# Kernel optimization log

Measured on AMD Instinct MI355X. Metric: run time of the kernel, lower is better.

The kernel has to match this reference:

```python
import jax, jax.numpy as jnp
import numpy as np

DEPTH = 4  # truncation depth of the signature


def setup_inputs() -> dict:
    key = jax.random.key(0)
    # path: (batch, stream, channels)
    path = jax.random.normal(key, (128, 128, 12), dtype=jnp.float32)
    return {"path": path}


def _exp_terms(d, depth):
    """Tensor exponential of a single linear increment d: (B, C).

    Returns a tuple of flattened levels; level k has shape (B, C**k) and
    equals d^{\otimes k} / k!.
    """
    B = d.shape[0]
    terms = [d]
    for k in range(2, depth + 1):
        terms.append(jnp.einsum('bi,bj->bij', terms[-1], d).reshape(B, -1) / k)
    return tuple(terms)


def _signature(path, depth):
    """Truncated path signature (stream=False, basepoint=False).

    Combines per-increment tensor exponentials with Chen's identity:
    (A \otimes B)_m = A_m + B_m + sum_{i=1}^{m-1} A_i \otimes B_{m-i}.
    """
    B, L, C = path.shape
    dx = path[:, 1:] - path[:, :-1]  # (B, L-1, C) path increments
    init = _exp_terms(dx[:, 0], depth)

    def step(sig, d):
        e = _exp_terms(d, depth)
        new = []
        for m in range(1, depth + 1):  # signature level m, shape (B, C**m)
            t = sig[m - 1] + e[m - 1]
            for i in range(1, m):  # cross terms sig_i (x) e_{m-i}
                t = t + jnp.einsum('bi,bj->bij', sig[i - 1], e[m - i - 1]).reshape(B, -1)
            new.append(t)
        return tuple(new), None

    # scan over the remaining L-2 increments (time-major)
    sig, _ = jax.lax.scan(step, init, jnp.transpose(dx[:, 1:], (1, 0, 2)))
    # flatten levels in order 1..depth, matching signatory's layout
    return jnp.concatenate(sig, axis=-1)  # (B, C + C^2 + ... + C^depth)


def reference(path):
    return _signature(path, DEPTH)
```

## Files before the change

kernel.cpp:

```cpp
#include <hip/hip_runtime.h>


#define NC    12
#define NPTS  128
#define NSTEP 128
#define OUT_PER_B 22620
#define BT 448
#define PADQ 33

__global__ __launch_bounds__(BT)
void sig_kernel(const float* __restrict__ path, float* __restrict__ out) {
    const int bid = blockIdx.x;
    const int b  = bid >> 1;
    const int ih = bid & 1;
    const int t  = threadIdx.x;

    __shared__ __align__(16) float  P[NPTS * NC];
    __shared__ __align__(16) float  W[NSTEP * NC];
    __shared__ __align__(16) float4 DT4[NC * PADQ];

    const float* pb = path + (size_t)b * (NPTS * NC);
    if (t < 384) ((float4*)P)[t] = ((const float4*)pb)[t];
    __syncthreads();

    if (t < 384) {
        const int c  = t >> 5;
        const int sq = t & 31;
        float d[4];
        #pragma unroll
        for (int e = 0; e < 4; ++e) {
            const int s = 4 * sq + e;
            d[e] = (s < NPTS - 1) ? (P[(s + 1) * NC + c] - P[s * NC + c]) : 0.f;
            W[s * NC + c] = d[e];
        }
        DT4[c * PADQ + sq] = make_float4(d[0], d[1], d[2], d[3]);
    }
    __syncthreads();

    const int ta  = (t < 432) ? t : (t - 432);
    const int il  = ta / 72;
    const int rem = ta - il * 72;
    const int j   = rem / 6;
    const int kh  = rem - j * 6;
    const int i   = ih * 6 + il;
    const int k0  = kh * 2;

    float acc0[12], acc1[12];
    #pragma unroll
    for (int l = 0; l < 12; ++l) { acc0[l] = 0.f; acc1[l] = 0.f; }
    float s3a = 0.f, s3b = 0.f, s2 = 0.f, s1 = 0.f;

    const float4* wt   = (const float4*)W;
    const float4* dti  = &DT4[i * PADQ];
    const float4* dtj  = &DT4[j * PADQ];
    const float4* dtka = &DT4[k0 * PADQ];
    const float4* dtkb = &DT4[(k0 + 1) * PADQ];

    for (int sq = 0; sq < NSTEP / 4; ++sq) {
        float4 wq[12];
        #pragma unroll
        for (int q = 0; q < 12; ++q) wq[q] = wt[sq * 12 + q];

        float4 di4  = dti[sq];
        float4 dj4  = dtj[sq];
        float4 dka4 = dtka[sq];
        float4 dkb4 = dtkb[sq];

        #pragma unroll
        for (int u = 0; u < 4; ++u) {
            const float di  = (&di4.x)[u];
            const float dj  = (&dj4.x)[u];
            const float dka = (&dka4.x)[u];
            const float dkb = (&dkb4.x)[u];

            float A4  = (s1 + 0.25f * di) * (1.f / 3.f);
            float B4  = (s2 + dj * A4) * 0.5f;
            float C3a = s3a + dka * B4;
            float C3b = s3b + dkb * B4;

            #pragma unroll
            for (int l = 0; l < 12; ++l) {
                const float wl = (&wq[3 * u + (l >> 2)].x)[l & 3];
                acc0[l] += C3a * wl;
                acc1[l] += C3b * wl;
            }

            float A3 = (s1 + di * (1.f / 3.f)) * 0.5f;
            float C2 = s2 + dj * A3;
            s3a += dka * C2;
            s3b += dkb * C2;
            s2  += dj * (s1 + 0.5f * di);
            s1  += di;
        }
    }

    if (t < 432) {
        float* ob = out + (size_t)b * OUT_PER_B;
        if (j == 0 && kh == 0) ob[i] = s1;
        if (kh == 0) ob[12 + i * 12 + j] = s2;
        const int ijk = (i * 12 + j) * 12 + k0;
        ob[156 + ijk]     = s3a;
        ob[156 + ijk + 1] = s3b;
        float4* o4 = (float4*)(ob + 1884 + (size_t)ijk * 12);
        o4[0] = make_float4(acc0[0], acc0[1], acc0[2],  acc0[3]);
        o4[1] = make_float4(acc0[4], acc0[5], acc0[6],  acc0[7]);
        o4[2] = make_float4(acc0[8], acc0[9], acc0[10], acc0[11]);
        o4[3] = make_float4(acc1[0], acc1[1], acc1[2],  acc1[3]);
        o4[4] = make_float4(acc1[4], acc1[5], acc1[6],  acc1[7]);
        o4[5] = make_float4(acc1[8], acc1[9], acc1[10], acc1[11]);
    }
}

extern "C" void kernel_launch(void* const* d_in, const int* in_sizes, int n_in,
                              void* d_out, int out_size, void* d_ws, size_t ws_size,
                              hipStream_t stream) {
    const float* path = (const float*)d_in[0];
    float* out = (float*)d_out;
    const int nbatch = in_sizes[0] / (NPTS * NC);

    sig_kernel<<<nbatch * 2, BT, 0, stream>>>(path, out);
}
```

Measured before the change: 73.47 us.

## Widen per-thread k tile to four and double-buffer shared-memory loads

Each thread now handles four k indices instead of two, so the block shrinks from 448 to 256 threads and each W/increment load from shared memory feeds twice as many FMAs. The step loop is manually double-buffered, prefetching the next quad of increments into registers while the current one is computed. The cost is much higher register pressure (48 accumulators plus two 12-float4 buffers), which may lower occupancy or cause spills. The longer serial chain per thread also leaves fewer waves to hide latency.

```diff
diff --git a/kernel.cpp b/kernel.cpp
--- a/kernel.cpp
+++ b/kernel.cpp
@@ -3,9 +3,8 @@
 
 #define NC    12
 #define NPTS  128
-#define NSTEP 128
 #define OUT_PER_B 22620
-#define BT 448
+#define BT 256
 #define PADQ 33
 
 __global__ __launch_bounds__(BT)
@@ -16,98 +15,128 @@
     const int t  = threadIdx.x;
 
     __shared__ __align__(16) float  P[NPTS * NC];
-    __shared__ __align__(16) float  W[NSTEP * NC];
+    __shared__ __align__(16) float  W[NPTS * NC];
     __shared__ __align__(16) float4 DT4[NC * PADQ];
 
-    const float* pb = path + (size_t)b * (NPTS * NC);
-    if (t < 384) ((float4*)P)[t] = ((const float4*)pb)[t];
-    __syncthreads();
-
-    if (t < 384) {
-        const int c  = t >> 5;
-        const int sq = t & 31;
-        float d[4];
-        #pragma unroll
-        for (int e = 0; e < 4; ++e) {
-            const int s = 4 * sq + e;
-            d[e] = (s < NPTS - 1) ? (P[(s + 1) * NC + c] - P[s * NC + c]) : 0.f;
-            W[s * NC + c] = d[e];
-        }
-        DT4[c * PADQ + sq] = make_float4(d[0], d[1], d[2], d[3]);
+    {
+        const float4* pb4 = (const float4*)(path + (size_t)b * (NPTS * NC));
+        ((float4*)P)[t] = pb4[t];
+        if (t < 128) ((float4*)P)[t + 256] = pb4[t + 256];
     }
     __syncthreads();
 
-    const int ta  = (t < 432) ? t : (t - 432);
-    const int il  = ta / 72;
-    const int rem = ta - il * 72;
-    const int j   = rem / 6;
-    const int kh  = rem - j * 6;
+    #pragma unroll
+    for (int pass = 0; pass < 2; ++pass) {
+        const int idx = t + pass * 256;
+        if (idx < 384) {
+            const int c  = idx >> 5;
+            const int sq = idx & 31;
+            float d[4];
+            #pragma unroll
+            for (int e = 0; e < 4; ++e) {
+                const int s = 4 * sq + e;
+                d[e] = (s < NPTS - 1) ? (P[(s + 1) * NC + c] - P[s * NC + c]) : 0.f;
+                W[s * NC + c] = d[e];
+            }
+            DT4[c * PADQ + sq] = make_float4(d[0], d[1], d[2], d[3]);
+        }
+    }
+    __syncthreads();
+
+    const int ta  = (t < 216) ? t : (t - 216);
+    const int il  = ta / 36;
+    const int rem = ta - il * 36;
+    const int j   = rem / 3;
+    const int kq  = rem - j * 3;
     const int i   = ih * 6 + il;
-    const int k0  = kh * 2;
+    const int k0  = kq * 4;
 
-    float acc0[12], acc1[12];
+    float acc[4][12];
     #pragma unroll
-    for (int l = 0; l < 12; ++l) { acc0[l] = 0.f; acc1[l] = 0.f; }
-    float s3a = 0.f, s3b = 0.f, s2 = 0.f, s1 = 0.f;
+    for (int m = 0; m < 4; ++m)
+        #pragma unroll
+        for (int l = 0; l < 12; ++l) acc[m][l] = 0.f;
+    float s1 = 0.f, s2 = 0.f;
+    float s3[4] = {0.f, 0.f, 0.f, 0.f};
 
     const float4* wt   = (const float4*)W;
     const float4* dti  = &DT4[i * PADQ];
     const float4* dtj  = &DT4[j * PADQ];
-    const float4* dtka = &DT4[k0 * PADQ];
-    const float4* dtkb = &DT4[(k0 + 1) * PADQ];
+    const float4* dtk0 = &DT4[(k0 + 0) * PADQ];
+    const float4* dtk1 = &DT4[(k0 + 1) * PADQ];
+    const float4* dtk2 = &DT4[(k0 + 2) * PADQ];
+    const float4* dtk3 = &DT4[(k0 + 3) * PADQ];
 
-    for (int sq = 0; sq < NSTEP / 4; ++sq) {
-        float4 wq[12];
-        #pragma unroll
-        for (int q = 0; q < 12; ++q) wq[q] = wt[sq * 12 + q];
+    float4 wqA[12], wqB[12];
+    float4 trA[6],  trB[6];
 
-        float4 di4  = dti[sq];
-        float4 dj4  = dtj[sq];
-        float4 dka4 = dtka[sq];
-        float4 dkb4 = dtkb[sq];
+#define LOADBUF(WQ, TR, S) do {                                   \
+        _Pragma("unroll")                                         \
+        for (int q = 0; q < 12; ++q) WQ[q] = wt[(S) * 12 + q];    \
+        TR[0] = dti[S];  TR[1] = dtj[S];                          \
+        TR[2] = dtk0[S]; TR[3] = dtk1[S];                         \
+        TR[4] = dtk2[S]; TR[5] = dtk3[S];                         \
+    } while (0)
 
-        #pragma unroll
-        for (int u = 0; u < 4; ++u) {
-            const float di  = (&di4.x)[u];
-            const float dj  = (&dj4.x)[u];
-            const float dka = (&dka4.x)[u];
-            const float dkb = (&dkb4.x)[u];
+#define COMPUTE(WQ, TR) do {                                      \
+        _Pragma("unroll")                                         \
+        for (int u = 0; u < 4; ++u) {                             \
+            const float di  = (&TR[0].x)[u];                      \
+            const float dj  = (&TR[1].x)[u];                      \
+            const float dk0_ = (&TR[2].x)[u];                     \
+            const float dk1_ = (&TR[3].x)[u];                     \
+            const float dk2_ = (&TR[4].x)[u];                     \
+            const float dk3_ = (&TR[5].x)[u];                     \
+            float A4 = (s1 + 0.25f * di) * (1.f / 3.f);           \
+            float B4 = (s2 + dj * A4) * 0.5f;                     \
+            float C3_0 = s3[0] + dk0_ * B4;                       \
+            float C3_1 = s3[1] + dk1_ * B4;                       \
+            float C3_2 = s3[2] + dk2_ * B4;                       \
+            float C3_3 = s3[3] + dk3_ * B4;                       \
+            _Pragma("unroll")                                     \
+            for (int l = 0; l < 12; ++l) {                        \
+                const float wl = (&WQ[3 * u + (l >> 2)].x)[l & 3];\
+                acc[0][l] += C3_0 * wl;                           \
+                acc[1][l] += C3_1 * wl;                           \
+                acc[2][l] += C3_2 * wl;                           \
+                acc[3][l] += C3_3 * wl;                           \
+            }                                                     \
+            float A3 = (s1 + di * (1.f / 3.f)) * 0.5f;            \
+            float C2 = s2 + dj * A3;                              \
+            s3[0] += dk0_ * C2;                                   \
+            s3[1] += dk1_ * C2;                                   \
+            s3[2] += dk2_ * C2;                                   \
+            s3[3] += dk3_ * C2;                                   \
+            s2 += dj * (s1 + 0.5f * di);                          \
+            s1 += di;                                             \
+        }                                                         \
+    } while (0)
 
-            float A4  = (s1 + 0.25f * di) * (1.f / 3.f);
-            float B4  = (s2 + dj * A4) * 0.5f;
-            float C3a = s3a + dka * B4;
-            float C3b = s3b + dkb * B4;
-
-            #pragma unroll
-            for (int l = 0; l < 12; ++l) {
-                const float wl = (&wq[3 * u + (l >> 2)].x)[l & 3];
-                acc0[l] += C3a * wl;
-                acc1[l] += C3b * wl;
-            }
-
-            float A3 = (s1 + di * (1.f / 3.f)) * 0.5f;
-            float C2 = s2 + dj * A3;
-            s3a += dka * C2;
-            s3b += dkb * C2;
-            s2  += dj * (s1 + 0.5f * di);
-            s1  += di;
-        }
+    LOADBUF(wqA, trA, 0);
+    for (int sq = 0; sq < 32; sq += 2) {
+        LOADBUF(wqB, trB, sq + 1);
+        COMPUTE(wqA, trA);
+        if (sq + 2 < 32) LOADBUF(wqA, trA, sq + 2);
+        COMPUTE(wqB, trB);
     }
 
-    if (t < 432) {
+#undef LOADBUF
+#undef COMPUTE
+
+    if (t < 216) {
         float* ob = out + (size_t)b * OUT_PER_B;
-        if (j == 0 && kh == 0) ob[i] = s1;
-        if (kh == 0) ob[12 + i * 12 + j] = s2;
+        if (j == 0 && kq == 0) ob[i] = s1;
+        if (kq == 0) ob[12 + i * 12 + j] = s2;
         const int ijk = (i * 12 + j) * 12 + k0;
-        ob[156 + ijk]     = s3a;
-        ob[156 + ijk + 1] = s3b;
+        *(float4*)(ob + 156 + ijk) =
+            make_float4(s3[0], s3[1], s3[2], s3[3]);
         float4* o4 = (float4*)(ob + 1884 + (size_t)ijk * 12);
-        o4[0] = make_float4(acc0[0], acc0[1], acc0[2],  acc0[3]);
-        o4[1] = make_float4(acc0[4], acc0[5], acc0[6],  acc0[7]);
-        o4[2] = make_float4(acc0[8], acc0[9], acc0[10], acc0[11]);
-        o4[3] = make_float4(acc1[0], acc1[1], acc1[2],  acc1[3]);
-        o4[4] = make_float4(acc1[4], acc1[5], acc1[6],  acc1[7]);
-        o4[5] = make_float4(acc1[8], acc1[9], acc1[10], acc1[11]);
+        #pragma unroll
+        for (int m = 0; m < 4; ++m) {
+            o4[m * 3 + 0] = make_float4(acc[m][0], acc[m][1], acc[m][2],  acc[m][3]);
+            o4[m * 3 + 1] = make_float4(acc[m][4], acc[m][5], acc[m][6],  acc[m][7]);
+            o4[m * 3 + 2] = make_float4(acc[m][8], acc[m][9], acc[m][10], acc[m][11]);
+        }
     }
 }
 
```

Measured after the change: 76.84 us. +4.6%, slower.

## Split time steps across two thread groups and merge halves via Chen identity

Applied to the files above, without the earlier changes.

Doubles the block to 896 threads and splits the 128 increments into two halves, each processed by its own group of 448 threads. The second-half group also computes the level-1..3 terms for the complementary i range, so that shared memory holds all the lower levels needed for the merge. The first group then combines both partial signatures with Chen's identity before writing out. This halves the serial dependency chain per thread, at the cost of more threads, extra shared memory (about 45KB for SB4), a block barrier, and extra merge arithmetic.

```diff
diff --git a/kernel.cpp b/kernel.cpp
--- a/kernel.cpp
+++ b/kernel.cpp
@@ -3,10 +3,10 @@
 
 #define NC    12
 #define NPTS  128
-#define NSTEP 128
 #define OUT_PER_B 22620
-#define BT 448
-#define PADQ 33
+#define BT    896
+#define PADQ  33
+#define SB4S  25
 
 __global__ __launch_bounds__(BT)
 void sig_kernel(const float* __restrict__ path, float* __restrict__ out) {
@@ -16,8 +16,12 @@
     const int t  = threadIdx.x;
 
     __shared__ __align__(16) float  P[NPTS * NC];
-    __shared__ __align__(16) float  W[NSTEP * NC];
+    __shared__ __align__(16) float  W[NPTS * NC];
     __shared__ __align__(16) float4 DT4[NC * PADQ];
+    __shared__ float SB1[12];
+    __shared__ float SB2[144];
+    __shared__ float SB3[1728];
+    __shared__ float SB4[432 * SB4S];
 
     const float* pb = path + (size_t)b * (NPTS * NC);
     if (t < 384) ((float4*)P)[t] = ((const float4*)pb)[t];
@@ -37,78 +41,135 @@
     }
     __syncthreads();
 
-    const int ta  = (t < 432) ? t : (t - 432);
+    const int g  = (t >= 448) ? 1 : 0;
+    const int tt = t - (g ? 448 : 0);
+    const int ta  = (tt < 432) ? tt : (tt - 432);
     const int il  = ta / 72;
     const int rem = ta - il * 72;
     const int j   = rem / 6;
     const int kh  = rem - j * 6;
     const int i   = ih * 6 + il;
+    const int ip  = (1 - ih) * 6 + il;
     const int k0  = kh * 2;
 
     float acc0[12], acc1[12];
     #pragma unroll
     for (int l = 0; l < 12; ++l) { acc0[l] = 0.f; acc1[l] = 0.f; }
-    float s3a = 0.f, s3b = 0.f, s2 = 0.f, s1 = 0.f;
+    float s1 = 0.f, s2 = 0.f, s3a = 0.f, s3b = 0.f;
+    float s1p = 0.f, s2p = 0.f, s3pa = 0.f, s3pb = 0.f;
 
     const float4* wt   = (const float4*)W;
     const float4* dti  = &DT4[i * PADQ];
     const float4* dtj  = &DT4[j * PADQ];
     const float4* dtka = &DT4[k0 * PADQ];
     const float4* dtkb = &DT4[(k0 + 1) * PADQ];
+    const float4* dtip = &DT4[ip * PADQ];
 
-    for (int sq = 0; sq < NSTEP / 4; ++sq) {
-        float4 wq[12];
-        #pragma unroll
-        for (int q = 0; q < 12; ++q) wq[q] = wt[sq * 12 + q];
+#define LOAD_COMMON(S)                                                \
+    float4 wq[12];                                                    \
+    _Pragma("unroll")                                                 \
+    for (int qq = 0; qq < 12; ++qq) wq[qq] = wt[(S) * 12 + qq];       \
+    float4 di4 = dti[S], dj4 = dtj[S], dka4 = dtka[S], dkb4 = dtkb[S];
 
-        float4 di4  = dti[sq];
-        float4 dj4  = dtj[sq];
-        float4 dka4 = dtka[sq];
-        float4 dkb4 = dtkb[sq];
+#define CHEN_U(u) do {                                                \
+        const float di  = (&di4.x)[u];                                \
+        const float dj  = (&dj4.x)[u];                                \
+        const float dka = (&dka4.x)[u];                               \
+        const float dkb = (&dkb4.x)[u];                               \
+        float A4  = (s1 + 0.25f * di) * (1.f / 3.f);                  \
+        float B4  = (s2 + dj * A4) * 0.5f;                            \
+        float C3a_ = s3a + dka * B4;                                  \
+        float C3b_ = s3b + dkb * B4;                                  \
+        _Pragma("unroll")                                             \
+        for (int l = 0; l < 12; ++l) {                                \
+            const float wl = (&wq[3 * u + (l >> 2)].x)[l & 3];        \
+            acc0[l] += C3a_ * wl;                                     \
+            acc1[l] += C3b_ * wl;                                     \
+        }                                                             \
+        float A3 = (s1 + di * (1.f / 3.f)) * 0.5f;                    \
+        float C2 = s2 + dj * A3;                                      \
+        s3a += dka * C2;                                              \
+        s3b += dkb * C2;                                              \
+        s2  += dj * (s1 + 0.5f * di);                                 \
+        s1  += di;                                                    \
+    } while (0)
 
-        #pragma unroll
-        for (int u = 0; u < 4; ++u) {
-            const float di  = (&di4.x)[u];
-            const float dj  = (&dj4.x)[u];
-            const float dka = (&dka4.x)[u];
-            const float dkb = (&dkb4.x)[u];
+#define CHEN_UP(u) do {                                               \
+        const float dip = (&dip4.x)[u];                               \
+        const float dj  = (&dj4.x)[u];                                \
+        const float dka = (&dka4.x)[u];                               \
+        const float dkb = (&dkb4.x)[u];                               \
+        float A3p = (s1p + dip * (1.f / 3.f)) * 0.5f;                 \
+        float C2p = s2p + dj * A3p;                                   \
+        s3pa += dka * C2p;                                            \
+        s3pb += dkb * C2p;                                            \
+        s2p  += dj * (s1p + 0.5f * dip);                              \
+        s1p  += dip;                                                  \
+    } while (0)
 
-            float A4  = (s1 + 0.25f * di) * (1.f / 3.f);
-            float B4  = (s2 + dj * A4) * 0.5f;
-            float C3a = s3a + dka * B4;
-            float C3b = s3b + dkb * B4;
-
+    if (!g) {
+        for (int q = 0; q < 16; ++q) {
+            LOAD_COMMON(q);
+            #pragma unroll
+            for (int u = 0; u < 4; ++u) CHEN_U(u);
+        }
+    } else {
+        for (int q = 16; q < 32; ++q) {
+            LOAD_COMMON(q);
+            float4 dip4 = dtip[q];
+            #pragma unroll
+            for (int u = 0; u < 4; ++u) { CHEN_U(u); CHEN_UP(u); }
+        }
+        if (tt < 432) {
             #pragma unroll
             for (int l = 0; l < 12; ++l) {
-                const float wl = (&wq[3 * u + (l >> 2)].x)[l & 3];
-                acc0[l] += C3a * wl;
-                acc1[l] += C3b * wl;
+                SB4[tt * SB4S + l]      = acc0[l];
+                SB4[tt * SB4S + 12 + l] = acc1[l];
             }
-
-            float A3 = (s1 + di * (1.f / 3.f)) * 0.5f;
-            float C2 = s2 + dj * A3;
-            s3a += dka * C2;
-            s3b += dkb * C2;
-            s2  += dj * (s1 + 0.5f * di);
-            s1  += di;
+            SB3[i  * 144 + j * 12 + k0]     = s3a;
+            SB3[i  * 144 + j * 12 + k0 + 1] = s3b;
+            SB3[ip * 144 + j * 12 + k0]     = s3pa;
+            SB3[ip * 144 + j * 12 + k0 + 1] = s3pb;
+            if (kh == 0) { SB2[i * 12 + j] = s2; SB2[ip * 12 + j] = s2p; }
+            if (j == 0 && kh == 0) { SB1[i] = s1; SB1[ip] = s1p; }
         }
     }
+    __syncthreads();
 
-    if (t < 432) {
+    if (!g && tt < 432) {
         float* ob = out + (size_t)b * OUT_PER_B;
-        if (j == 0 && kh == 0) ob[i] = s1;
-        if (kh == 0) ob[12 + i * 12 + j] = s2;
+        if (j == 0 && kh == 0) ob[i] = s1 + SB1[i];
+        if (kh == 0)
+            ob[12 + i * 12 + j] = s2 + SB2[i * 12 + j] + s1 * SB1[j];
         const int ijk = (i * 12 + j) * 12 + k0;
-        ob[156 + ijk]     = s3a;
-        ob[156 + ijk + 1] = s3b;
+        ob[156 + ijk] = s3a + SB3[i * 144 + j * 12 + k0]
+                      + s1 * SB2[j * 12 + k0] + s2 * SB1[k0];
+        ob[156 + ijk + 1] = s3b + SB3[i * 144 + j * 12 + k0 + 1]
+                      + s1 * SB2[j * 12 + k0 + 1] + s2 * SB1[k0 + 1];
+        float c4[24];
+        #pragma unroll
+        for (int l = 0; l < 12; ++l) {
+            c4[l] = acc0[l] + SB4[tt * SB4S + l]
+                  + s1 * SB3[j * 144 + k0 * 12 + l]
+                  + s2 * SB2[k0 * 12 + l]
+                  + s3a * SB1[l];
+            c4[12 + l] = acc1[l] + SB4[tt * SB4S + 12 + l]
+                  + s1 * SB3[j * 144 + (k0 + 1) * 12 + l]
+                  + s2 * SB2[(k0 + 1) * 12 + l]
+                  + s3b * SB1[l];
+        }
         float4* o4 = (float4*)(ob + 1884 + (size_t)ijk * 12);
-        o4[0] = make_float4(acc0[0], acc0[1], acc0[2],  acc0[3]);
-        o4[1] = make_float4(acc0[4], acc0[5], acc0[6],  acc0[7]);
-        o4[2] = make_float4(acc0[8], acc0[9], acc0[10], acc0[11]);
-        o4[3] = make_float4(acc1[0], acc1[1], acc1[2],  acc1[3]);
-        o4[4] = make_float4(acc1[4], acc1[5], acc1[6],  acc1[7]);
-        o4[5] = make_float4(acc1[8], acc1[9], acc1[10], acc1[11]);
+        o4[0] = make_float4(c4[0],  c4[1],  c4[2],  c4[3]);
+        o4[1] = make_float4(c4[4],  c4[5],  c4[6],  c4[7]);
+        o4[2] = make_float4(c4[8],  c4[9],  c4[10], c4[11]);
+        o4[3] = make_float4(c4[12], c4[13], c4[14], c4[15]);
+        o4[4] = make_float4(c4[16], c4[17], c4[18], c4[19]);
+        o4[5] = make_float4(c4[20], c4[21], c4[22], c4[23]);
     }
+
+#undef LOAD_COMMON
+#undef CHEN_U
+#undef CHEN_UP
 }
 
 extern "C" void kernel_launch(void* const* d_in, const int* in_sizes, int n_in,
```

After: 79.49 us. +8.2%, slower.
